# Kernel optimization log

Measured on AMD Instinct MI355X. Metric: run time of the kernel, lower is better.

## Reference

```python
import jax, jax.numpy as jnp
import numpy as np

N_HEAD = 16
N_KV_HEAD = 4
WINDOW = 256
ROPE_BASE = 10000.0


def _rotate_half(x):
    h = x.shape[-1] // 2
    return jnp.concatenate([-x[..., h:], x[..., :h]], axis=-1)


def _rope_cos_sin(T, D):
    inv_freq = 1.0 / (ROPE_BASE ** (jnp.arange(0, D, 2, dtype=jnp.float32) / D))
    t = jnp.arange(T, dtype=jnp.float32)
    freqs = t[:, None] * inv_freq[None, :]            # [T, D/2]
    emb = jnp.concatenate([freqs, freqs], axis=-1)    # [T, D]
    return jnp.cos(emb)[None, None], jnp.sin(emb)[None, None]  # [1,1,T,D]


def _masks(T, w):
    tq = jnp.arange(T)
    tk = jnp.arange(T)
    causal = tk[None, :] <= tq[:, None]
    i_blk = (tq // w) * w                              # window block start per query
    k_start = jnp.maximum(0, i_blk - w // 2)           # local key slice start
    # torch SDPA is_causal with L!=S: top-left aligned tril -> local kj <= local qi
    upper = tq - (i_blk - k_start)
    local = (tk[None, :] >= k_start[:, None]) & (tk[None, :] <= upper[:, None])
    return causal, local


def setup_inputs() -> dict:
    key = jax.random.key(0)
    k0, k1, k2, k3, k4 = jax.random.split(key, 5)
    B, T, C = 1, 2048, 2048
    D = C // N_HEAD
    s = 0.02
    return {
        "x": jax.random.normal(k0, (B, T, C), dtype=jnp.float32),
        "wq": jax.random.normal(k1, (C, N_HEAD * D), dtype=jnp.float32) * s,
        "wk": jax.random.normal(k2, (C, N_KV_HEAD * D), dtype=jnp.float32) * s,
        "wv": jax.random.normal(k3, (C, N_KV_HEAD * D), dtype=jnp.float32) * s,
        "wo": jax.random.normal(k4, (C, C), dtype=jnp.float32) * s,
    }


def reference(x, wq, wk, wv, wo):
    B, T, C = x.shape
    D = C // N_HEAD
    g = N_HEAD // N_KV_HEAD

    q = (x @ wq).reshape(B, T, N_HEAD, D)
    k = (x @ wk).reshape(B, T, N_KV_HEAD, D)
    v = (x @ wv).reshape(B, T, N_KV_HEAD, D)
    k = jnp.repeat(k, g, axis=2)                       # GQA repeat_interleave
    v = jnp.repeat(v, g, axis=2)
    q = q.transpose(0, 2, 1, 3)                        # [B,H,T,D]
    k = k.transpose(0, 2, 1, 3)
    v = v.transpose(0, 2, 1, 3)

    cos, sin = _rope_cos_sin(T, D)
    q = q * cos + _rotate_half(q) * sin
    k = k * cos + _rotate_half(k) * sin

    scale = 1.0 / jnp.sqrt(jnp.asarray(D, dtype=q.dtype))
    scores = jnp.einsum('bhqd,bhkd->bhqk', q, k) * scale
    causal, local = _masks(T, WINDOW)
    neg = jnp.finfo(scores.dtype).min
    p_g = jax.nn.softmax(jnp.where(causal, scores, neg), axis=-1)
    p_l = jax.nn.softmax(jnp.where(local, scores, neg), axis=-1)
    out_g = jnp.einsum('bhqk,bhkd->bhqd', p_g, v)
    out_l = jnp.einsum('bhqk,bhkd->bhqd', p_l, v)
    out = 0.5 * (out_g + out_l)
    out = out.transpose(0, 2, 1, 3).reshape(B, T, C)
    return out @ wo
```

## Files before the change

### kernel.cpp

```cpp
#include <hip/hip_runtime.h>
#include <hip/hip_bf16.h>
#include <cstdint>
#include <cstddef>

#define T_SEQ 2048
#define CDIM  2048
#define HQ    16
#define HKV   4
#define DHEAD 128
#define NQKV  3072

typedef __bf16 bf8 __attribute__((ext_vector_type(8)));
typedef __bf16 bf4 __attribute__((ext_vector_type(4)));
typedef float  f4  __attribute__((ext_vector_type(4)));

static __device__ __forceinline__ f4 mfma16(bf8 a, bf8 b, f4 c) {
    return __builtin_amdgcn_mfma_f32_16x16x32_bf16(a, b, c, 0, 0, 0);
}

#define GLOAD16(g, l)                                                        \
    __builtin_amdgcn_global_load_lds(                                        \
        (const __attribute__((address_space(1))) void*)(g),                  \
        (__attribute__((address_space(3))) void*)(l), 16, 0, 0)

__global__ __launch_bounds__(256) void k_pre(const float* __restrict__ x,
                                             const float* __restrict__ wq,
                                             const float* __restrict__ wk,
                                             const float* __restrict__ wv,
                                             const float* __restrict__ wo,
                                             __bf16* __restrict__ xbf,
                                             float* __restrict__ tab,
                                             __bf16* __restrict__ wqkvT,
                                             __bf16* __restrict__ woT) {
    const int bid = blockIdx.x, tid = threadIdx.x;
    if (bid < 4096) {
        int i = bid * 256 + tid;
        float4 v = ((const float4*)x)[i];
        bf4 o;
        o[0] = (__bf16)v.x; o[1] = (__bf16)v.y; o[2] = (__bf16)v.z; o[3] = (__bf16)v.w;
        ((bf4*)xbf)[i] = o;
        return;
    }
    if (bid < 4608) {
        int idx = (bid - 4096) * 256 + tid;
        int t = idx >> 6, j = idx & 63;
        float invf = expf(-(float)j * (9.210340371976184f / 64.0f));
        float a = (float)t * invf;
        tab[idx * 2 + 0] = cosf(a);
        tab[idx * 2 + 1] = sinf(a);
        return;
    }
    __shared__ float tile[32][33];
    const int n = bid - 4608;
    const int bx = n % 160, by = n / 160;
    const float* src; __bf16* dst; int ld_src, cx;
    if (bx < 64)      { src = wq; dst = wqkvT;                        ld_src = 2048; cx = bx; }
    else if (bx < 80) { src = wk; dst = wqkvT + (size_t)2048 * 2048;  ld_src = 512;  cx = bx - 64; }
    else if (bx < 96) { src = wv; dst = wqkvT + (size_t)2560 * 2048;  ld_src = 512;  cx = bx - 80; }
    else              { src = wo; dst = woT;                          ld_src = 2048; cx = bx - 96; }
    const int c0 = cx * 32, r0 = by * 32;
    const int tx = tid & 31, ty = tid >> 5;
#pragma unroll
    for (int i = 0; i < 4; ++i)
        tile[ty + i * 8][tx] = src[(size_t)(r0 + ty + i * 8) * ld_src + c0 + tx];
    __syncthreads();
#pragma unroll
    for (int i = 0; i < 4; ++i)
        dst[(size_t)(c0 + ty + i * 8) * 2048 + r0 + tx] = (__bf16)tile[tx][ty + i * 8];
}

template <int MODE>
__global__ __launch_bounds__(512, 4) void k_gemm(const __bf16* __restrict__ A,
                                                 const __bf16* __restrict__ BT,
                                                 float* __restrict__ C,
                                                 const float2* __restrict__ tab,
                                                 __bf16* __restrict__ Qo,
                                                 __bf16* __restrict__ Ko,
                                                 __bf16* __restrict__ Vo,
                                                 int M, int N, int K) {
    __shared__ __bf16 lds[2][2][128 * 64];
    char* L = (char*)&lds[0][0][0];
    const int tid = threadIdx.x, wid = tid >> 6, lane = tid & 63;
    const int l15 = lane & 15, lhi = lane >> 4;
    const int wr = wid >> 1, wc = wid & 1;
    const size_t arow0 = (size_t)blockIdx.y * 128;
    const size_t brow0 = (size_t)blockIdx.x * 128;

    const int sr = tid >> 3;
    const int sc8 = ((tid & 7) ^ ((tid >> 3) & 7)) * 8;
    const __bf16* Ag = A + (arow0 + sr) * K + sc8;
    const __bf16* Bg = BT + (brow0 + sr) * K + sc8;

#define GSTAGE(buf, k0)                                                          \
    {                                                                            \
        _Pragma("unroll") for (int i = 0; i < 2; ++i) {                          \
            GLOAD16(Ag + (k0) + (size_t)i * 64 * K,                              \
                    L + (buf) * 32768 + i * 8192 + tid * 16);                    \
            GLOAD16(Bg + (k0) + (size_t)i * 64 * K,                              \
                    L + (buf) * 32768 + 16384 + i * 8192 + tid * 16);            \
        }                                                                        \
    }

    f4 acc[2][4] = {};
    GSTAGE(0, 0);
    __syncthreads();
    int cur = 0;

    for (int k0 = 0; k0 < K; k0 += 64) {
        if (k0 + 64 < K) GSTAGE(cur ^ 1, k0 + 64);
        const char* Ab = L + cur * 32768;
        const char* Bb = Ab + 16384;
        bf8 af[2][2], bfr[2][4];
#pragma unroll
        for (int kk = 0; kk < 2; ++kk) {
            const int ch = ((kk * 4 + lhi) ^ (l15 & 7)) * 16;
#pragma unroll
            for (int m = 0; m < 2; ++m)
                af[kk][m] = *(const bf8*)(Ab + (wr * 32 + m * 16 + l15) * 128 + ch);
#pragma unroll
            for (int n = 0; n < 4; ++n)
                bfr[kk][n] = *(const bf8*)(Bb + (n * 32 + wc * 16 + l15) * 128 + ch);
        }
#pragma unroll
        for (int kk = 0; kk < 2; ++kk)
#pragma unroll
            for (int m = 0; m < 2; ++m)
#pragma unroll
                for (int n = 0; n < 4; ++n)
                    acc[m][n] = mfma16(af[kk][m], bfr[kk][n], acc[m][n]);
        __syncthreads();
        cur ^= 1;
    }
#undef GSTAGE

    const int row0 = blockIdx.y * 128 + wr * 32;
    if (MODE == 0) {
#pragma unroll
        for (int m = 0; m < 2; ++m)
#pragma unroll
            for (int n = 0; n < 4; ++n) {
                const int c = blockIdx.x * 128 + n * 32 + wc * 16 + l15;
#pragma unroll
                for (int j = 0; j < 4; ++j)
                    C[(size_t)(row0 + m * 16 + lhi * 4 + j) * N + c] = acc[m][n][j];
            }
    } else {
        const int bx = blockIdx.x;
        if (bx < 20) {
            __bf16* dst0 = (bx < 16) ? (Qo + (size_t)bx * T_SEQ * DHEAD)
                                     : (Ko + (size_t)(bx - 16) * T_SEQ * DHEAD);
#pragma unroll
            for (int m = 0; m < 2; ++m)
#pragma unroll
                for (int n = 0; n < 2; ++n) {
                    const int d = n * 32 + wc * 16 + l15;
#pragma unroll
                    for (int j = 0; j < 4; ++j) {
                        const int t = row0 + m * 16 + lhi * 4 + j;
                        const float2 cs = tab[t * 64 + d];
                        const float a = acc[m][n][j], b = acc[m][n + 2][j];
                        dst0[(size_t)t * DHEAD + d]      = (__bf16)(a * cs.x - b * cs.y);
                        dst0[(size_t)t * DHEAD + d + 64] = (__bf16)(b * cs.x + a * cs.y);
                    }
                }
        } else {
            __bf16* vdst = Vo + (size_t)(bx - 20) * DHEAD * T_SEQ;
#pragma unroll
            for (int m = 0; m < 2; ++m)
#pragma unroll
                for (int n = 0; n < 4; ++n) {
                    const int c = n * 32 + wc * 16 + l15;
                    bf4 o;
#pragma unroll
                    for (int j = 0; j < 4; ++j) o[j] = (__bf16)acc[m][n][j];
                    *(bf4*)&vdst[(size_t)c * T_SEQ + row0 + m * 16 + lhi * 4] = o;
                }
        }
    }
}

__global__ __launch_bounds__(512) void k_attn(const __bf16* __restrict__ Q,
                                              const __bf16* __restrict__ Kr,
                                              const __bf16* __restrict__ VT,
                                              __bf16* __restrict__ att) {
    __shared__ __align__(16) char lds[155648];
    char* KlB  = lds;
    char* VlB  = lds + 65536;
    char* PlB0 = lds + 131072;
    char* PwB0 = lds + 147456;

    const int h = blockIdx.y, kvh = h >> 2;
    const int qt = (blockIdx.y < 8) ? (31 - (int)blockIdx.x) : (int)blockIdx.x;
    const int tid = threadIdx.x, wid = tid >> 6, lane = tid & 63;
    const int l15 = lane & 15, lhi = lane >> 4;
    const int par = wid >> 2, qw = wid & 3;
    const int q0w = qt * 64 + qw * 16;
    const bool hasloc = qt >= 4;
    const int lfLo = 4 * (qt >> 2) - 2;
    const int lpart = qt - 2;
    const float CE = 0.12751741f;
    const float L2E = 1.44269504f;
    const float SCL = 0.08838834764831845f;
    const float THR = 5.5451774f;

    char* PlB = PlB0 + wid * 2048;
    char* PwB = PwB0 + qw * 2048;

    const int srow = tid >> 4;
    const int sg = (((tid & 15) ^ (srow & 15)) << 3);
    const __bf16* KgB = Kr + (size_t)kvh * T_SEQ * DHEAD;
    const __bf16* VgB = VT + (size_t)kvh * DHEAD * T_SEQ;

#define STAGE(bsel, kb2)                                                          \
    {                                                                             \
        _Pragma("unroll") for (int i = 0; i < 4; ++i) {                           \
            GLOAD16(KgB + (size_t)((kb2) + i * 32 + srow) * DHEAD + sg,           \
                    KlB + (bsel) + i * 8192 + tid * 16);                          \
            GLOAD16(VgB + (size_t)(i * 32 + srow) * T_SEQ + (kb2) + sg,           \
                    VlB + (bsel) + i * 8192 + tid * 16);                          \
        }                                                                         \
    }

    bf8 qf[4];
#pragma unroll
    for (int dc = 0; dc < 4; ++dc)
        qf[dc] = *(const bf8*)&Q[((size_t)h * T_SEQ + q0w + l15) * DHEAD + dc * 32 + lhi * 8];

    f4 oc[8] = {}, ow[8] = {};
    float mg[4], sgp[4], slp[4];
#pragma unroll
    for (int j = 0; j < 4; ++j) { mg[j] = -__builtin_inff(); sgp[j] = slp[j] = 0.f; }
    float mgmin = -__builtin_inff();

    const int R = (qt >> 1) + 1;
    STAGE(0, 0);
    __syncthreads();
    int cur = 0;

    for (int r = 0; r < R; ++r) {
        if (r + 1 < R) STAGE((cur ^ 1) * 32768, (r + 1) * 128);
        const int kt = 2 * r + par;
        if (kt <= qt) {
            const int kb = kt * 64;
            const int cb = cur * 32768;
            const int rowb = par * 64;
            f4 sc[4] = {};
#pragma unroll
            for (int ks = 0; ks < 4; ++ks)
#pragma unroll
                for (int dc = 0; dc < 4; ++dc) {
                    bf8 kf = *(const bf8*)(KlB + cb + (rowb + ks * 16 + l15) * 256 +
                                           (((dc * 4 + lhi) ^ l15) << 4));
                    sc[ks] = mfma16(qf[dc], kf, sc[ks]);
                }

            float t[4][4];
#pragma unroll
            for (int ks = 0; ks < 4; ++ks)
#pragma unroll
                for (int j = 0; j < 4; ++j) t[ks][j] = sc[ks][j];
            if (kt == qt) {
#pragma unroll
                for (int ks = 0; ks < 4; ++ks)
#pragma unroll
                    for (int j = 0; j < 4; ++j)
                        if (kb + ks * 16 + l15 > q0w + lhi * 4 + j) t[ks][j] = -3.0e38f;
            }
            float mx = t[0][0];
#pragma unroll
            for (int ks = 0; ks < 4; ++ks)
#pragma unroll
                for (int j = 0; j < 4; ++j) mx = fmaxf(mx, t[ks][j]);
            mx *= SCL;
            if (!__all(mx <= mgmin + THR)) {
#pragma unroll
                for (int j = 0; j < 4; ++j) {
                    float m2 = fmaxf(fmaxf(t[0][j], t[1][j]), fmaxf(t[2][j], t[3][j])) * SCL;
#pragma unroll
                    for (int x = 1; x < 16; x <<= 1) m2 = fmaxf(m2, __shfl_xor(m2, x));
                    float mn = fmaxf(mg[j], m2);
                    float f = __builtin_amdgcn_exp2f((mg[j] - mn) * L2E);
                    mg[j] = mn;
                    sgp[j] *= f; slp[j] *= f;
#pragma unroll
                    for (int nd = 0; nd < 8; ++nd) { oc[nd][j] *= f; ow[nd][j] *= f; }
                }
                mgmin = fminf(fminf(mg[0], mg[1]), fminf(mg[2], mg[3]));
            }
            float p[4][4], psum[4];
#pragma unroll
            for (int j = 0; j < 4; ++j) {
                const float bj = mg[j] * L2E;
#pragma unroll
                for (int ks = 0; ks < 4; ++ks)
                    p[ks][j] = __builtin_amdgcn_exp2f(t[ks][j] * CE - bj);
                psum[j] = (p[0][j] + p[1][j]) + (p[2][j] + p[3][j]);
                sgp[j] += psum[j];
            }
            const bool part = hasloc && (kt == lpart);
            if (!part) {
#pragma unroll
                for (int j = 0; j < 4; ++j) {
                    const int rsw = ((lhi * 4 + j) & 7) << 4;
                    const int rb = (lhi * 4 + j) * 128;
#pragma unroll
                    for (int ks = 0; ks < 4; ++ks)
                        *(__bf16*)(PlB + rb + ((ks * 32 + 2 * l15) ^ rsw)) = (__bf16)p[ks][j];
                }
            } else {
                const int e = q0w + lhi * 4 - 128 - kb - l15;
#pragma unroll
                for (int j = 0; j < 4; ++j) {
                    const int rsw = ((lhi * 4 + j) & 7) << 4;
                    const int rb = (lhi * 4 + j) * 128;
                    float lsum = 0.f;
#pragma unroll
                    for (int ks = 0; ks < 4; ++ks) {
                        float l = (ks * 16 <= e + j) ? p[ks][j] : 0.f;
                        lsum += l;
                        *(__bf16*)(PwB + rb + ((ks * 32 + 2 * l15) ^ rsw)) = (__bf16)l;
                        *(__bf16*)(PlB + rb + ((ks * 32 + 2 * l15) ^ rsw)) = (__bf16)(p[ks][j] - l);
                    }
                    slp[j] += lsum;
                }
            }
            const bool inwin = hasloc && kt >= lfLo && kt < lpart;
            if (inwin) {
#pragma unroll
                for (int j = 0; j < 4; ++j) slp[j] += psum[j];
            }
            const int psw = (l15 & 7) << 4;
            bf8 pf0 = *(const bf8*)(PlB + l15 * 128 + ((lhi << 4) ^ psw));
            bf8 pf1 = *(const bf8*)(PlB + l15 * 128 + ((64 + (lhi << 4)) ^ psw));
            const int vg0 = ((par * 8 + lhi) ^ l15) << 4;
            const int vg1 = ((par * 8 + 4 + lhi) ^ l15) << 4;
            if (part) {
                bf8 pw0 = *(const bf8*)(PwB + l15 * 128 + ((lhi << 4) ^ psw));
                bf8 pw1 = *(const bf8*)(PwB + l15 * 128 + ((64 + (lhi << 4)) ^ psw));
#pragma unroll
                for (int nd = 0; nd < 8; ++nd) {
                    bf8 v0 = *(const bf8*)(VlB + cb + (nd * 16 + l15) * 256 + vg0);
                    bf8 v1 = *(const bf8*)(VlB + cb + (nd * 16 + l15) * 256 + vg1);
                    oc[nd] = mfma16(pf0, v0, oc[nd]);
                    oc[nd] = mfma16(pf1, v1, oc[nd]);
                    ow[nd] = mfma16(pw0, v0, ow[nd]);
                    ow[nd] = mfma16(pw1, v1, ow[nd]);
                }
            } else if (inwin) {
#pragma unroll
                for (int nd = 0; nd < 8; ++nd) {
                    bf8 v0 = *(const bf8*)(VlB + cb + (nd * 16 + l15) * 256 + vg0);
                    bf8 v1 = *(const bf8*)(VlB + cb + (nd * 16 + l15) * 256 + vg1);
                    ow[nd] = mfma16(pf0, v0, ow[nd]);
                    ow[nd] = mfma16(pf1, v1, ow[nd]);
                }
            } else {
#pragma unroll
                for (int nd = 0; nd < 8; ++nd) {
                    bf8 v0 = *(const bf8*)(VlB + cb + (nd * 16 + l15) * 256 + vg0);
                    bf8 v1 = *(const bf8*)(VlB + cb + (nd * 16 + l15) * 256 + vg1);
                    oc[nd] = mfma16(pf0, v0, oc[nd]);
                    oc[nd] = mfma16(pf1, v1, oc[nd]);
                }
            }
        }
        __syncthreads();
        cur ^= 1;
    }

    char* sb = lds + (size_t)(qw * 64 + lane) * 16;
    if (par) {
#pragma unroll
        for (int nd = 0; nd < 8; ++nd) *(f4*)(sb + nd * 4096) = oc[nd];
#pragma unroll
        for (int nd = 0; nd < 8; ++nd) *(f4*)(sb + (8 + nd) * 4096) = ow[nd];
        f4 a, b, c;
#pragma unroll
        for (int j = 0; j < 4; ++j) { a[j] = mg[j]; b[j] = sgp[j]; c[j] = slp[j]; }
        *(f4*)(sb + 16 * 4096) = a; *(f4*)(sb + 17 * 4096) = b; *(f4*)(sb + 18 * 4096) = c;
    }
    __syncthreads();
    if (!par) {
        f4 mB = *(const f4*)(sb + 16 * 4096);
        f4 sB = *(const f4*)(sb + 17 * 4096);
        f4 lB = *(const f4*)(sb + 18 * 4096);
        float fA[4], fB[4];
#pragma unroll
        for (int j = 0; j < 4; ++j) {
            float ms = fmaxf(mg[j], mB[j]);
            fA[j] = __builtin_amdgcn_exp2f((mg[j] - ms) * L2E);
            fB[j] = __builtin_amdgcn_exp2f((mB[j] - ms) * L2E);
            sgp[j] = sgp[j] * fA[j] + sB[j] * fB[j];
            slp[j] = slp[j] * fA[j] + lB[j] * fB[j];
        }
#pragma unroll
        for (int nd = 0; nd < 8; ++nd) {
            f4 ocB = *(const f4*)(sb + nd * 4096);
            f4 owB = *(const f4*)(sb + (8 + nd) * 4096);
#pragma unroll
            for (int j = 0; j < 4; ++j) {
                oc[nd][j] = oc[nd][j] * fA[j] + ocB[j] * fB[j];
                ow[nd][j] = ow[nd][j] * fA[j] + owB[j] * fB[j];
            }
        }
#pragma unroll
        for (int j = 0; j < 4; ++j) {
#pragma unroll
            for (int x = 1; x < 16; x <<= 1) {
                sgp[j] += __shfl_xor(sgp[j], x);
                slp[j] += __shfl_xor(slp[j], x);
            }
        }
        float rg[4], rl[4];
#pragma unroll
        for (int j = 0; j < 4; ++j) {
            rg[j] = 1.f / sgp[j];
            rl[j] = hasloc ? 0.5f / slp[j] : 0.f;
        }
#pragma unroll
        for (int nd = 0; nd < 8; ++nd)
#pragma unroll
            for (int j = 0; j < 4; ++j) {
                int q = q0w + lhi * 4 + j;
                float go = oc[nd][j] + ow[nd][j];
                float v = hasloc ? (go * (0.5f * rg[j]) + ow[nd][j] * rl[j]) : go * rg[j];
                att[(size_t)q * CDIM + h * DHEAD + nd * 16 + l15] = (__bf16)v;
            }
    }
#undef STAGE
}

extern "C" void kernel_launch(void* const* d_in, const int* in_sizes, int n_in,
                              void* d_out, int out_size, void* d_ws, size_t ws_size,
                              hipStream_t stream) {
    const float* x  = (const float*)d_in[0];
    const float* wq = (const float*)d_in[1];
    const float* wk = (const float*)d_in[2];
    const float* wv = (const float*)d_in[3];
    const float* wo = (const float*)d_in[4];
    char* ws = (char*)d_ws;

    __bf16* xbf   = (__bf16*)(ws + 0);
    __bf16* wqkvT = (__bf16*)(ws + 8388608);
    __bf16* woT   = (__bf16*)(ws + 20971520);
    __bf16* Q     = (__bf16*)(ws + 41943040);
    __bf16* K     = (__bf16*)(ws + 50331648);
    __bf16* VTb   = (__bf16*)(ws + 52428800);
    __bf16* att   = (__bf16*)(ws + 54525952);
    float*  tab   = (float*)(ws + 62914560);

    k_pre<<<14848, 256, 0, stream>>>(x, wq, wk, wv, wo, xbf, tab, wqkvT, woT);
    k_gemm<1><<<dim3(24, 16), 512, 0, stream>>>(xbf, wqkvT, nullptr, (const float2*)tab,
                                                Q, K, VTb, 2048, 3072, 2048);
    k_attn<<<dim3(32, 16), 512, 0, stream>>>(Q, K, VTb, att);
    k_gemm<0><<<dim3(16, 16), 512, 0, stream>>>(att, woT, (float*)d_out, nullptr,
                                                nullptr, nullptr, nullptr, 2048, 2048, 2048);
}
```

Baseline: 137.6 us.

## Split attention key tiles across four waves per query group with 1024-thread blocks

The attention kernel now launches 1024 threads per block. Each of four wave groups takes a 32-key sub-tile of every 128-key stage, where before two groups each took 64 keys, so each wave does half the per-step work and more waves run concurrently. The separate window-P buffer is dropped by reusing the per-wave P buffer, and the four partial softmax states are merged through LDS in a chain of barriers. This adds more syncs and merge traffic, uses more registers per block under launch_bounds(1024), and guards merges against -inf maxima.

Result: slower. 314.6 us (+128.6%).

```diff
diff --git a/kernel.cpp b/kernel.cpp
--- a/kernel.cpp
+++ b/kernel.cpp
@@ -179,15 +179,14 @@
     }
 }
 
-__global__ __launch_bounds__(512) void k_attn(const __bf16* __restrict__ Q,
-                                              const __bf16* __restrict__ Kr,
-                                              const __bf16* __restrict__ VT,
-                                              __bf16* __restrict__ att) {
-    __shared__ __align__(16) char lds[155648];
+__global__ __launch_bounds__(1024, 4) void k_attn(const __bf16* __restrict__ Q,
+                                                  const __bf16* __restrict__ Kr,
+                                                  const __bf16* __restrict__ VT,
+                                                  __bf16* __restrict__ att) {
+    __shared__ __align__(16) char lds[147456];
     char* KlB  = lds;
     char* VlB  = lds + 65536;
     char* PlB0 = lds + 131072;
-    char* PwB0 = lds + 147456;
 
     const int h = blockIdx.y, kvh = h >> 2;
     const int qt = (blockIdx.y < 8) ? (31 - (int)blockIdx.x) : (int)blockIdx.x;
@@ -196,28 +195,27 @@
     const int par = wid >> 2, qw = wid & 3;
     const int q0w = qt * 64 + qw * 16;
     const bool hasloc = qt >= 4;
-    const int lfLo = 4 * (qt >> 2) - 2;
-    const int lpart = qt - 2;
+    const int dt = 2 * qt + (qw >> 1);
+    const int pt = 2 * qt - 4 + (qw >> 1);
+    const int lfLo32 = 8 * (qt >> 2) - 4;
     const float CE = 0.12751741f;
     const float L2E = 1.44269504f;
     const float SCL = 0.08838834764831845f;
     const float THR = 5.5451774f;
 
-    char* PlB = PlB0 + wid * 2048;
-    char* PwB = PwB0 + qw * 2048;
-
-    const int srow = tid >> 4;
-    const int sg = (((tid & 15) ^ (srow & 15)) << 3);
+    char* PlB = PlB0 + wid * 1024;
+
+    const int sg = (((tid & 15) ^ ((tid >> 4) & 15)) << 3);
     const __bf16* KgB = Kr + (size_t)kvh * T_SEQ * DHEAD;
     const __bf16* VgB = VT + (size_t)kvh * DHEAD * T_SEQ;
 
 #define STAGE(bsel, kb2)                                                          \
     {                                                                             \
-        _Pragma("unroll") for (int i = 0; i < 4; ++i) {                           \
-            GLOAD16(KgB + (size_t)((kb2) + i * 32 + srow) * DHEAD + sg,           \
-                    KlB + (bsel) + i * 8192 + tid * 16);                          \
-            GLOAD16(VgB + (size_t)(i * 32 + srow) * T_SEQ + (kb2) + sg,           \
-                    VlB + (bsel) + i * 8192 + tid * 16);                          \
+        _Pragma("unroll") for (int i = 0; i < 2; ++i) {                           \
+            GLOAD16(KgB + (size_t)((kb2) + i * 64 + (tid >> 4)) * DHEAD + sg,     \
+                    KlB + (bsel) + i * 16384 + tid * 16);                         \
+            GLOAD16(VgB + (size_t)(i * 64 + (tid >> 4)) * T_SEQ + (kb2) + sg,     \
+                    VlB + (bsel) + i * 16384 + tid * 16);                         \
         }                                                                         \
     }
 
@@ -239,14 +237,14 @@
 
     for (int r = 0; r < R; ++r) {
         if (r + 1 < R) STAGE((cur ^ 1) * 32768, (r + 1) * 128);
-        const int kt = 2 * r + par;
-        if (kt <= qt) {
-            const int kb = kt * 64;
+        const int kt = 4 * r + par;
+        if (kt <= dt) {
+            const int kb = kt * 32;
             const int cb = cur * 32768;
-            const int rowb = par * 64;
-            f4 sc[4] = {};
-#pragma unroll
-            for (int ks = 0; ks < 4; ++ks)
+            const int rowb = par * 32;
+            f4 sc[2] = {};
+#pragma unroll
+            for (int ks = 0; ks < 2; ++ks)
 #pragma unroll
                 for (int dc = 0; dc < 4; ++dc) {
                     bf8 kf = *(const bf8*)(KlB + cb + (rowb + ks * 16 + l15) * 256 +
@@ -254,32 +252,30 @@
                     sc[ks] = mfma16(qf[dc], kf, sc[ks]);
                 }
 
-            float t[4][4];
-#pragma unroll
-            for (int ks = 0; ks < 4; ++ks)
+            float t[2][4];
+#pragma unroll
+            for (int ks = 0; ks < 2; ++ks)
 #pragma unroll
                 for (int j = 0; j < 4; ++j) t[ks][j] = sc[ks][j];
-            if (kt == qt) {
-#pragma unroll
-                for (int ks = 0; ks < 4; ++ks)
+            if (kt == dt) {
+#pragma unroll
+                for (int ks = 0; ks < 2; ++ks)
 #pragma unroll
                     for (int j = 0; j < 4; ++j)
                         if (kb + ks * 16 + l15 > q0w + lhi * 4 + j) t[ks][j] = -3.0e38f;
             }
-            float mx = t[0][0];
-#pragma unroll
-            for (int ks = 0; ks < 4; ++ks)
-#pragma unroll
-                for (int j = 0; j < 4; ++j) mx = fmaxf(mx, t[ks][j]);
+            float mx = fmaxf(t[0][0], t[1][0]);
+#pragma unroll
+            for (int j = 1; j < 4; ++j) mx = fmaxf(mx, fmaxf(t[0][j], t[1][j]));
             mx *= SCL;
             if (!__all(mx <= mgmin + THR)) {
 #pragma unroll
                 for (int j = 0; j < 4; ++j) {
-                    float m2 = fmaxf(fmaxf(t[0][j], t[1][j]), fmaxf(t[2][j], t[3][j])) * SCL;
+                    float m2 = fmaxf(t[0][j], t[1][j]) * SCL;
 #pragma unroll
                     for (int x = 1; x < 16; x <<= 1) m2 = fmaxf(m2, __shfl_xor(m2, x));
                     float mn = fmaxf(mg[j], m2);
-                    float f = __builtin_amdgcn_exp2f((mg[j] - mn) * L2E);
+                    float f = __builtin_amdgcn_exp2f((fmaxf(mg[j], -1.0e30f) - mn) * L2E);
                     mg[j] = mn;
                     sgp[j] *= f; slp[j] *= f;
 #pragma unroll
@@ -287,80 +283,71 @@
                 }
                 mgmin = fminf(fminf(mg[0], mg[1]), fminf(mg[2], mg[3]));
             }
-            float p[4][4], psum[4];
+            float p[2][4], psum[4];
 #pragma unroll
             for (int j = 0; j < 4; ++j) {
                 const float bj = mg[j] * L2E;
-#pragma unroll
-                for (int ks = 0; ks < 4; ++ks)
-                    p[ks][j] = __builtin_amdgcn_exp2f(t[ks][j] * CE - bj);
-                psum[j] = (p[0][j] + p[1][j]) + (p[2][j] + p[3][j]);
+                p[0][j] = __builtin_amdgcn_exp2f(t[0][j] * CE - bj);
+                p[1][j] = __builtin_amdgcn_exp2f(t[1][j] * CE - bj);
+                psum[j] = p[0][j] + p[1][j];
                 sgp[j] += psum[j];
             }
-            const bool part = hasloc && (kt == lpart);
-            if (!part) {
+            const bool part = hasloc && (kt == pt);
+            const bool inwin = hasloc && kt >= lfLo32 && kt < pt;
+            const int e = q0w + lhi * 4 - 128 - kb - l15;
+#pragma unroll
+            for (int j = 0; j < 4; ++j) {
+                const int row = lhi * 4 + j;
+                const int rsw = ((row >> 2) & 3) << 4;
+                float lsum = 0.f;
+#pragma unroll
+                for (int ks = 0; ks < 2; ++ks) {
+                    float v = p[ks][j];
+                    if (part) {
+                        float l = (ks * 16 <= e + j) ? v : 0.f;
+                        lsum += l;
+                        v -= l;
+                    }
+                    *(__bf16*)(PlB + row * 64 + ((ks * 32 + 2 * l15) ^ rsw)) = (__bf16)v;
+                }
+                if (part) slp[j] += lsum;
+            }
+            if (inwin) {
+#pragma unroll
+                for (int j = 0; j < 4; ++j) slp[j] += psum[j];
+            }
+            const int psw = ((l15 >> 2) & 3) << 4;
+            bf8 pf0 = *(const bf8*)(PlB + l15 * 64 + ((lhi << 4) ^ psw));
+            const int vg = ((par * 4 + lhi) ^ l15) << 4;
+            if (part) {
 #pragma unroll
                 for (int j = 0; j < 4; ++j) {
-                    const int rsw = ((lhi * 4 + j) & 7) << 4;
-                    const int rb = (lhi * 4 + j) * 128;
-#pragma unroll
-                    for (int ks = 0; ks < 4; ++ks)
-                        *(__bf16*)(PlB + rb + ((ks * 32 + 2 * l15) ^ rsw)) = (__bf16)p[ks][j];
+                    const int row = lhi * 4 + j;
+                    const int rsw = ((row >> 2) & 3) << 4;
+#pragma unroll
+                    for (int ks = 0; ks < 2; ++ks) {
+                        float l = (ks * 16 <= e + j) ? p[ks][j] : 0.f;
+                        *(__bf16*)(PlB + row * 64 + ((ks * 32 + 2 * l15) ^ rsw)) = (__bf16)l;
+                    }
+                }
+                bf8 pw0 = *(const bf8*)(PlB + l15 * 64 + ((lhi << 4) ^ psw));
+#pragma unroll
+                for (int nd = 0; nd < 8; ++nd) {
+                    bf8 v0 = *(const bf8*)(VlB + cb + (nd * 16 + l15) * 256 + vg);
+                    oc[nd] = mfma16(pf0, v0, oc[nd]);
+                    ow[nd] = mfma16(pw0, v0, ow[nd]);
+                }
+            } else if (inwin) {
+#pragma unroll
+                for (int nd = 0; nd < 8; ++nd) {
+                    bf8 v0 = *(const bf8*)(VlB + cb + (nd * 16 + l15) * 256 + vg);
+                    ow[nd] = mfma16(pf0, v0, ow[nd]);
                 }
             } else {
-                const int e = q0w + lhi * 4 - 128 - kb - l15;
-#pragma unroll
-                for (int j = 0; j < 4; ++j) {
-                    const int rsw = ((lhi * 4 + j) & 7) << 4;
-                    const int rb = (lhi * 4 + j) * 128;
-                    float lsum = 0.f;
-#pragma unroll
-                    for (int ks = 0; ks < 4; ++ks) {
-                        float l = (ks * 16 <= e + j) ? p[ks][j] : 0.f;
-                        lsum += l;
-                        *(__bf16*)(PwB + rb + ((ks * 32 + 2 * l15) ^ rsw)) = (__bf16)l;
-                        *(__bf16*)(PlB + rb + ((ks * 32 + 2 * l15) ^ rsw)) = (__bf16)(p[ks][j] - l);
-                    }
-                    slp[j] += lsum;
-                }
-            }
-            const bool inwin = hasloc && kt >= lfLo && kt < lpart;
-            if (inwin) {
-#pragma unroll
-                for (int j = 0; j < 4; ++j) slp[j] += psum[j];
-            }
-            const int psw = (l15 & 7) << 4;
-            bf8 pf0 = *(const bf8*)(PlB + l15 * 128 + ((lhi << 4) ^ psw));
-            bf8 pf1 = *(const bf8*)(PlB + l15 * 128 + ((64 + (lhi << 4)) ^ psw));
-            const int vg0 = ((par * 8 + lhi) ^ l15) << 4;
-            const int vg1 = ((par * 8 + 4 + lhi) ^ l15) << 4;
-            if (part) {
-                bf8 pw0 = *(const bf8*)(PwB + l15 * 128 + ((lhi << 4) ^ psw));
-                bf8 pw1 = *(const bf8*)(PwB + l15 * 128 + ((64 + (lhi << 4)) ^ psw));
 #pragma unroll
                 for (int nd = 0; nd < 8; ++nd) {
-                    bf8 v0 = *(const bf8*)(VlB + cb + (nd * 16 + l15) * 256 + vg0);
-                    bf8 v1 = *(const bf8*)(VlB + cb + (nd * 16 + l15) * 256 + vg1);
+                    bf8 v0 = *(const bf8*)(VlB + cb + (nd * 16 + l15) * 256 + vg);
                     oc[nd] = mfma16(pf0, v0, oc[nd]);
-                    oc[nd] = mfma16(pf1, v1, oc[nd]);
-                    ow[nd] = mfma16(pw0, v0, ow[nd]);
-                    ow[nd] = mfma16(pw1, v1, ow[nd]);
-                }
-            } else if (inwin) {
-#pragma unroll
-                for (int nd = 0; nd < 8; ++nd) {
-                    bf8 v0 = *(const bf8*)(VlB + cb + (nd * 16 + l15) * 256 + vg0);
-                    bf8 v1 = *(const bf8*)(VlB + cb + (nd * 16 + l15) * 256 + vg1);
-                    ow[nd] = mfma16(pf0, v0, ow[nd]);
-                    ow[nd] = mfma16(pf1, v1, ow[nd]);
-                }
-            } else {
-#pragma unroll
-                for (int nd = 0; nd < 8; ++nd) {
-                    bf8 v0 = *(const bf8*)(VlB + cb + (nd * 16 + l15) * 256 + vg0);
-                    bf8 v1 = *(const bf8*)(VlB + cb + (nd * 16 + l15) * 256 + vg1);
-                    oc[nd] = mfma16(pf0, v0, oc[nd]);
-                    oc[nd] = mfma16(pf1, v1, oc[nd]);
                 }
             }
         }
@@ -369,7 +356,7 @@
     }
 
     char* sb = lds + (size_t)(qw * 64 + lane) * 16;
-    if (par) {
+    auto writeState = [&]() {
 #pragma unroll
         for (int nd = 0; nd < 8; ++nd) *(f4*)(sb + nd * 4096) = oc[nd];
 #pragma unroll
@@ -378,20 +365,21 @@
 #pragma unroll
         for (int j = 0; j < 4; ++j) { a[j] = mg[j]; b[j] = sgp[j]; c[j] = slp[j]; }
         *(f4*)(sb + 16 * 4096) = a; *(f4*)(sb + 17 * 4096) = b; *(f4*)(sb + 18 * 4096) = c;
-    }
-    __syncthreads();
-    if (!par) {
+    };
+    auto mergeState = [&]() {
         f4 mB = *(const f4*)(sb + 16 * 4096);
         f4 sB = *(const f4*)(sb + 17 * 4096);
         f4 lB = *(const f4*)(sb + 18 * 4096);
         float fA[4], fB[4];
 #pragma unroll
         for (int j = 0; j < 4; ++j) {
-            float ms = fmaxf(mg[j], mB[j]);
-            fA[j] = __builtin_amdgcn_exp2f((mg[j] - ms) * L2E);
-            fB[j] = __builtin_amdgcn_exp2f((mB[j] - ms) * L2E);
+            float cA = fmaxf(mg[j], -1.0e30f), cB = fmaxf(mB[j], -1.0e30f);
+            float ms = fmaxf(cA, cB);
+            fA[j] = __builtin_amdgcn_exp2f((cA - ms) * L2E);
+            fB[j] = __builtin_amdgcn_exp2f((cB - ms) * L2E);
             sgp[j] = sgp[j] * fA[j] + sB[j] * fB[j];
             slp[j] = slp[j] * fA[j] + lB[j] * fB[j];
+            mg[j] = fmaxf(mg[j], mB[j]);
         }
 #pragma unroll
         for (int nd = 0; nd < 8; ++nd) {
@@ -403,6 +391,16 @@
                 ow[nd][j] = ow[nd][j] * fA[j] + owB[j] * fB[j];
             }
         }
+    };
+    __syncthreads();
+    if (par == 3) writeState();
+    __syncthreads();
+    if (par == 2) { mergeState(); writeState(); }
+    __syncthreads();
+    if (par == 1) { mergeState(); writeState(); }
+    __syncthreads();
+    if (par == 0) {
+        mergeState();
 #pragma unroll
         for (int j = 0; j < 4; ++j) {
 #pragma unroll
@@ -452,7 +450,7 @@
     k_pre<<<14848, 256, 0, stream>>>(x, wq, wk, wv, wo, xbf, tab, wqkvT, woT);
     k_gemm<1><<<dim3(24, 16), 512, 0, stream>>>(xbf, wqkvT, nullptr, (const float2*)tab,
                                                 Q, K, VTb, 2048, 3072, 2048);
-    k_attn<<<dim3(32, 16), 512, 0, stream>>>(Q, K, VTb, att);
+    k_attn<<<dim3(32, 16), 1024, 0, stream>>>(Q, K, VTb, att);
     k_gemm<0><<<dim3(16, 16), 512, 0, stream>>>(att, woT, (float*)d_out, nullptr,
                                                 nullptr, nullptr, nullptr, 2048, 2048, 2048);
 }
```
